# Kernel optimization log

Measured on AMD Instinct MI355X. Metric: run time of the kernel, lower is better.

Reference implementation:

```python
import jax, jax.numpy as jnp
import numpy as np


def setup_inputs() -> dict:
    key = jax.random.key(0)
    ks = jax.random.split(key, 6)
    B, E, N, F = 512, 4, 256, 64
    node = jax.random.normal(ks[0], (B, N, F), dtype=jnp.float32)
    adj = jax.random.uniform(ks[1], (B, E, N, N), dtype=jnp.float32)
    s = 1.0 / np.sqrt(F)
    W_edge = jax.random.uniform(ks[2], (E, F, F), dtype=jnp.float32, minval=-s, maxval=s)
    b_edge = jax.random.uniform(ks[3], (E, F), dtype=jnp.float32, minval=-s, maxval=s)
    W_add = jax.random.uniform(ks[4], (F, F), dtype=jnp.float32, minval=-s, maxval=s)
    b_add = jax.random.uniform(ks[5], (F,), dtype=jnp.float32, minval=-s, maxval=s)
    return {"node": node, "adj": adj, "W_edge": W_edge, "b_edge": b_edge,
            "W_add": W_add, "b_add": b_add}


def reference(node, adj, W_edge, b_edge, W_add, b_add):
    # per-edge-type linear: [B,N,F_in] x [E,F_in,F_out] -> [B,E,N,F_out]
    hidden = jnp.einsum('bnf,efg->beng', node, W_edge) + b_edge[None, :, None, :]
    # adjacency-weighted aggregation per edge type: [B,E,N,N] @ [B,E,N,F_out]
    msg = jnp.einsum('benm,bemg->beng', adj, hidden)
    # sum over edge types + residual linear (dropout=0, activation=None)
    out = jnp.sum(msg, axis=1) + node @ W_add + b_add
    return out
```

## Files before the change

kernel.cpp:

```cpp
#include <hip/hip_runtime.h>

typedef __attribute__((ext_vector_type(8))) short short8;
typedef __attribute__((ext_vector_type(4))) float f32x4;

#define MFMA16(a, b, c) __builtin_amdgcn_mfma_f32_16x16x32_bf16((a), (b), (c), 0, 0, 0)

static __device__ inline short f2bf(float x) {
    union { float f; unsigned u; } v;
    v.f = x;
    unsigned r = v.u + 0x7fffu + ((v.u >> 16) & 1u);
    return (short)(r >> 16);
}
static __device__ inline short4 f2bf4(float4 v) {
    short4 s;
    s.x = f2bf(v.x); s.y = f2bf(v.y); s.z = f2bf(v.z); s.w = f2bf(v.w);
    return s;
}

__global__ __launch_bounds__(256, 2) void gconv_kernel(
    const float* __restrict__ node,
    const float* __restrict__ adj,
    const float* __restrict__ W_edge,
    const float* __restrict__ b_edge,
    const float* __restrict__ W_add,
    const float* __restrict__ b_add,
    float* __restrict__ out)
{
    __shared__ short adjL[64][264];
    __shared__ short hiddenT[64][264];
    __shared__ short wT[64][72];
    const int b    = blockIdx.x;
    const int t    = threadIdx.x;
    const int lane = t & 63;
    const int w    = t >> 6;
    const int col  = lane & 15;
    const int kq   = lane >> 4;

    const float* nodeB = node + (size_t)b * (256 * 64);
    const float* adjB  = adj  + (size_t)b * (4 * 256 * 256);

    short8 anode[4][2];
    #pragma unroll
    for (int st = 0; st < 4; ++st)
        #pragma unroll
        for (int h = 0; h < 2; ++h) {
            const float* p = nodeB + (st * 64 + 16 * w + col) * 64 + 32 * h + 8 * kq;
            float4 v0 = *(const float4*)p;
            float4 v1 = *(const float4*)(p + 4);
            short8 a;
            a[0] = f2bf(v0.x); a[1] = f2bf(v0.y); a[2] = f2bf(v0.z); a[3] = f2bf(v0.w);
            a[4] = f2bf(v1.x); a[5] = f2bf(v1.y); a[6] = f2bf(v1.z); a[7] = f2bf(v1.w);
            anode[st][h] = a;
        }

    float4 v[16];
    {
        const float* s0 = adjB + t * 4;
        #pragma unroll
        for (int i = 0; i < 16; ++i)
            v[i] = *(const float4*)(s0 + i * 1024);
    }

    #pragma unroll
    for (int i = 0; i < 16; ++i) {
        int idx = i * 256 + t;
        wT[idx & 63][idx >> 6] = f2bf(W_add[idx]);
    }
    __syncthreads();

    f32x4 acc[4][4];
    {
        const f32x4 zf = {0.f, 0.f, 0.f, 0.f};
        #pragma unroll
        for (int st = 0; st < 4; ++st)
            #pragma unroll
            for (int ct = 0; ct < 4; ++ct)
                acc[st][ct] = zf;
        #pragma unroll
        for (int h = 0; h < 2; ++h) {
            short8 bfr[4];
            #pragma unroll
            for (int ct = 0; ct < 4; ++ct)
                bfr[ct] = *(const short8*)&wT[16 * ct + col][32 * h + 8 * kq];
            #pragma unroll
            for (int st = 0; st < 4; ++st)
                #pragma unroll
                for (int ct = 0; ct < 4; ++ct)
                    acc[st][ct] = MFMA16(anode[st][h], bfr[ct], acc[st][ct]);
        }
    }
    __syncthreads();

    for (int e = 0; e < 4; ++e) {
        const float* We = W_edge + e * (64 * 64);
        #pragma unroll
        for (int i = 0; i < 16; ++i) {
            int idx = i * 256 + t;
            wT[idx & 63][idx >> 6] = f2bf(We[idx]);
        }
        float bedge[4];
        #pragma unroll
        for (int ct = 0; ct < 4; ++ct)
            bedge[ct] = b_edge[e * 64 + 16 * ct + col];
        __syncthreads();

        #pragma unroll
        for (int ct = 0; ct < 4; ++ct) {
            short8 b0 = *(const short8*)&wT[16 * ct + col][8 * kq];
            short8 b1 = *(const short8*)&wT[16 * ct + col][32 + 8 * kq];
            #pragma unroll
            for (int st = 0; st < 4; ++st) {
                f32x4 h = {0.f, 0.f, 0.f, 0.f};
                h = MFMA16(anode[st][0], b0, h);
                h = MFMA16(anode[st][1], b1, h);
                short4 s;
                s.x = f2bf(h[0] + bedge[ct]); s.y = f2bf(h[1] + bedge[ct]);
                s.z = f2bf(h[2] + bedge[ct]); s.w = f2bf(h[3] + bedge[ct]);
                *(short4*)&hiddenT[16 * ct + col][st * 64 + 16 * w + 4 * kq] = s;
            }
        }
        __syncthreads();

        #pragma unroll
        for (int mt = 0; mt < 4; ++mt) {
            #pragma unroll
            for (int i = 0; i < 16; ++i)
                *(short4*)&adjL[4 * i + w][4 * lane] = f2bf4(v[i]);

            int p = e * 4 + mt;
            if (p < 15) {
                const float* s0 = adjB + (size_t)(p + 1) * 16384 + t * 4;
                #pragma unroll
                for (int i = 0; i < 16; ++i)
                    v[i] = *(const float4*)(s0 + i * 1024);
            }
            __syncthreads();

            #pragma unroll
            for (int ks = 0; ks < 8; ++ks) {
                short8 af = *(const short8*)&adjL[16 * w + col][32 * ks + 8 * kq];
                #pragma unroll
                for (int ct = 0; ct < 4; ++ct) {
                    short8 bf = *(const short8*)&hiddenT[16 * ct + col][32 * ks + 8 * kq];
                    acc[mt][ct] = MFMA16(af, bf, acc[mt][ct]);
                }
            }
            __syncthreads();
        }
    }

    float* outB = out + (size_t)b * (256 * 64);
    #pragma unroll
    for (int ct = 0; ct < 4; ++ct) {
        float bias = b_add[16 * ct + col];
        #pragma unroll
        for (int st = 0; st < 4; ++st) {
            int row = st * 64 + 16 * w + 4 * kq;
            #pragma unroll
            for (int r = 0; r < 4; ++r)
                outB[(size_t)(row + r) * 64 + 16 * ct + col] = acc[st][ct][r] + bias;
        }
    }
}

extern "C" void kernel_launch(void* const* d_in, const int* in_sizes, int n_in,
                              void* d_out, int out_size, void* d_ws, size_t ws_size,
                              hipStream_t stream) {
    const float* node   = (const float*)d_in[0];
    const float* adj    = (const float*)d_in[1];
    const float* W_edge = (const float*)d_in[2];
    const float* b_edge = (const float*)d_in[3];
    const float* W_add  = (const float*)d_in[4];
    const float* b_add  = (const float*)d_in[5];
    float* out = (float*)d_out;

    gconv_kernel<<<dim3(512), dim3(256), 0, stream>>>(
        node, adj, W_edge, b_edge, W_add, b_add, out);
}
```

Before: 710.7 us.

## Load adjacency MFMA fragments directly from global memory, dropping LDS staging

Removes the shared-memory adjacency tile and its register prefetch buffer. Each wave now loads its own adjacency row fragments straight from global memory into MFMA A-operands, converting to bf16 in registers. This drops two barriers per tile and the LDS write/read round trip, and frees LDS and registers. In exchange, the loads are less coalesced (each lane reads 32 contiguous bytes per step), there is no explicit prefetch across tiles, and the partial unroll may leave memory latency exposed.

After: 721.5 us. Within noise of the previous version (+1.5%).

```diff
diff --git a/kernel.cpp b/kernel.cpp
--- a/kernel.cpp
+++ b/kernel.cpp
@@ -11,11 +11,6 @@
     unsigned r = v.u + 0x7fffu + ((v.u >> 16) & 1u);
     return (short)(r >> 16);
 }
-static __device__ inline short4 f2bf4(float4 v) {
-    short4 s;
-    s.x = f2bf(v.x); s.y = f2bf(v.y); s.z = f2bf(v.z); s.w = f2bf(v.w);
-    return s;
-}
 
 __global__ __launch_bounds__(256, 2) void gconv_kernel(
     const float* __restrict__ node,
@@ -26,7 +21,6 @@
     const float* __restrict__ b_add,
     float* __restrict__ out)
 {
-    __shared__ short adjL[64][264];
     __shared__ short hiddenT[64][264];
     __shared__ short wT[64][72];
     const int b    = blockIdx.x;
@@ -52,14 +46,6 @@
             a[4] = f2bf(v1.x); a[5] = f2bf(v1.y); a[6] = f2bf(v1.z); a[7] = f2bf(v1.w);
             anode[st][h] = a;
         }
-
-    float4 v[16];
-    {
-        const float* s0 = adjB + t * 4;
-        #pragma unroll
-        for (int i = 0; i < 16; ++i)
-            v[i] = *(const float4*)(s0 + i * 1024);
-    }
 
     #pragma unroll
     for (int i = 0; i < 16; ++i) {
@@ -91,6 +77,7 @@
     }
     __syncthreads();
 
+    #pragma unroll 1
     for (int e = 0; e < 4; ++e) {
         const float* We = W_edge + e * (64 * 64);
         #pragma unroll
@@ -121,31 +108,25 @@
         }
         __syncthreads();
 
+        const float* aRow = adjB + e * (256 * 256) + (16 * w + col) * 256 + 8 * kq;
         #pragma unroll
         for (int mt = 0; mt < 4; ++mt) {
-            #pragma unroll
-            for (int i = 0; i < 16; ++i)
-                *(short4*)&adjL[4 * i + w][4 * lane] = f2bf4(v[i]);
-
-            int p = e * 4 + mt;
-            if (p < 15) {
-                const float* s0 = adjB + (size_t)(p + 1) * 16384 + t * 4;
-                #pragma unroll
-                for (int i = 0; i < 16; ++i)
-                    v[i] = *(const float4*)(s0 + i * 1024);
-            }
-            __syncthreads();
-
-            #pragma unroll
+            const float* ap = aRow + mt * (64 * 256);
+            #pragma unroll 2
             for (int ks = 0; ks < 8; ++ks) {
-                short8 af = *(const short8*)&adjL[16 * w + col][32 * ks + 8 * kq];
+                float4 v0 = *(const float4*)(ap + 32 * ks);
+                float4 v1 = *(const float4*)(ap + 32 * ks + 4);
+                short8 af;
+                af[0] = f2bf(v0.x); af[1] = f2bf(v0.y);
+                af[2] = f2bf(v0.z); af[3] = f2bf(v0.w);
+                af[4] = f2bf(v1.x); af[5] = f2bf(v1.y);
+                af[6] = f2bf(v1.z); af[7] = f2bf(v1.w);
                 #pragma unroll
                 for (int ct = 0; ct < 4; ++ct) {
                     short8 bf = *(const short8*)&hiddenT[16 * ct + col][32 * ks + 8 * kq];
                     acc[mt][ct] = MFMA16(af, bf, acc[mt][ct]);
                 }
             }
-            __syncthreads();
         }
     }
 
```
